# Kernel optimization log

Hardware: AMD Instinct MI355X
Metric: run time of the kernel (lower is better)

Reference implementation:

```python
import jax, jax.numpy as jnp
import numpy as np

B, T, D, H, DEPTH, FF, NC = 512, 150, 256, 8, 6, 1024, 4
HD = D // H  # head dim = 32


def setup_inputs() -> dict:
    key = jax.random.key(0)
    ks = iter(jax.random.split(key, 64))
    n = lambda shape, s=0.02: jax.random.normal(next(ks), shape, jnp.float32) * s
    return dict(
        token_types=jax.random.randint(next(ks), (B, T), 0, 4, jnp.int32),
        decision_ids=jax.random.randint(next(ks), (B, T), 0, NC, jnp.int32),
        action_vals=jax.random.normal(next(ks), (B, T, 1), jnp.float32),
        dis_vals=jax.random.normal(next(ks), (B, T, 10), jnp.float32),
        v_vals=jax.random.normal(next(ks), (B, T, 3), jnp.float32),
        action_W=n((1, D), 0.5), action_b=n((D,)),
        dis_W=n((10, D), 0.2), dis_b=n((D,)),
        v_W=n((3, D), 0.3), v_b=n((D,)),
        decision_table=n((NC, D)),
        pos_embed=n((1, T + 1, D)), cls_token=n((1, 1, D)),
        qkv_W=n((DEPTH, D, 3 * D), 0.05), qkv_b=jnp.zeros((DEPTH, 3 * D), jnp.float32),
        out_W=n((DEPTH, D, D), 0.05), out_b=jnp.zeros((DEPTH, D), jnp.float32),
        ln1_g=jnp.ones((DEPTH, D), jnp.float32), ln1_b=jnp.zeros((DEPTH, D), jnp.float32),
        ln2_g=jnp.ones((DEPTH, D), jnp.float32), ln2_b=jnp.zeros((DEPTH, D), jnp.float32),
        ffn1_W=n((DEPTH, D, FF), 0.05), ffn1_b=jnp.zeros((DEPTH, FF), jnp.float32),
        ffn2_W=n((DEPTH, FF, D), 0.05), ffn2_b=jnp.zeros((DEPTH, D), jnp.float32),
        dec_ln_g=jnp.ones((D,), jnp.float32), dec_ln_b=jnp.zeros((D,), jnp.float32),
        dec_W=n((D, NC), 0.05), dec_b=jnp.zeros((NC,), jnp.float32),
        act_ln_g=jnp.ones((D,), jnp.float32), act_ln_b=jnp.zeros((D,), jnp.float32),
        act_W=n((D, 1), 0.05), act_b=jnpp if False else jnp.zeros((1,), jnp.float32),
    )


def _ln(x, g, b):
    # PyTorch LayerNorm: eps=1e-5, biased variance
    m = jnp.mean(x, axis=-1, keepdims=True)
    v = jnp.mean(jnp.square(x - m), axis=-1, keepdims=True)
    return (x - m) * jax.lax.rsqrt(v + 1e-5) * g + b


def reference(token_types, decision_ids, action_vals, dis_vals, v_vals,
              action_W, action_b, dis_W, dis_b, v_W, v_b, decision_table,
              pos_embed, cls_token, qkv_W, qkv_b, out_W, out_b,
              ln1_g, ln1_b, ln2_g, ln2_b, ffn1_W, ffn1_b, ffn2_W, ffn2_b,
              dec_ln_g, dec_ln_b, dec_W, dec_b, act_ln_g, act_ln_b, act_W, act_b):
    # --- batched type-dispatched token embedding (replaces the per-token python loop) ---
    a_emb = action_vals @ action_W + action_b                     # [B,T,D] type 'A'
    s_emb = dis_vals @ dis_W + dis_b + v_vals @ v_W + v_b         # [B,T,D] type 'S'
    d_emb = decision_table[decision_ids]                          # [B,T,D] type 'D'
    t = token_types[..., None]
    x = jnp.where(t == 0, a_emb, jnp.where(t == 1, s_emb, jnp.where(t == 2, d_emb, 0.0)))
    # --- prepend CLS, add positional embedding ---
    x = jnp.concatenate([jnp.broadcast_to(cls_token, (x.shape[0], 1, D)), x], axis=1)
    S = x.shape[1]
    x = x + pos_embed[:, :S, :]
    # --- post-norm TransformerEncoder (PyTorch default: ReLU FFN, norm_first=False, eval/no dropout) ---
    scale = 1.0 / np.sqrt(HD).astype(np.float32)
    for i in range(DEPTH):
        qkv = x @ qkv_W[i] + qkv_b[i]                             # [B,S,3D]
        q, k, v = jnp.split(qkv, 3, axis=-1)
        q = q.reshape(-1, S, H, HD)
        k = k.reshape(-1, S, H, HD)
        v = v.reshape(-1, S, H, HD)
        att = jax.nn.softmax(jnp.einsum('bqhd,bkhd->bhqk', q, k) * scale, axis=-1)
        o = jnp.einsum('bhqk,bkhd->bqhd', att, v).reshape(-1, S, D)
        x = _ln(x + o @ out_W[i] + out_b[i], ln1_g[i], ln1_b[i])
        ff = jax.nn.relu(x @ ffn1_W[i] + ffn1_b[i]) @ ffn2_W[i] + ffn2_b[i]
        x = _ln(x + ff, ln2_g[i], ln2_b[i])
    cls = x[:, 0, :]
    decision_logits = _ln(cls, dec_ln_g, dec_ln_b) @ dec_W + dec_b   # [B,4]
    action_pred = _ln(cls, act_ln_g, act_ln_b) @ act_W + act_b       # [B,1]
    return (decision_logits, action_pred)
```

## Files before the change

kernel.cpp:

```cpp
#include <hip/hip_runtime.h>
#include <hip/hip_bf16.h>

typedef __hip_bfloat16 bf16;
typedef unsigned short u16;
typedef __attribute__((ext_vector_type(8))) short s16x8;
typedef __attribute__((ext_vector_type(4))) float f32x4;

#define B_ 512
#define T_ 150
#define S_ 151
#define D_ 256
#define H_ 8
#define HD_ 32
#define FF_ 1024
#define NC_ 4
#define DEPTH_ 6
#define MTOT 77312
#define MT128 (MTOT / 128)
#define MT64 (MTOT / 64)

#define XOFF 0
#define C1OFF (MTOT * D_)
#define C2OFF (C1OFF + MTOT * FF_)
#define WSELEMS (C2OFF + MTOT * D_)

#define QKVT_OFF 0
#define OUTT_OFF (QKVT_OFF + DEPTH_ * D_ * 768)
#define FFN1T_OFF (OUTT_OFF + DEPTH_ * D_ * D_)
#define FFN2T_OFF (FFN1T_OFF + DEPTH_ * D_ * FF_)
#define WTELEMS (FFN2T_OFF + DEPTH_ * FF_ * D_)

__device__ __align__(16) u16 g_ws[WSELEMS];
__device__ __align__(16) u16 g_wt[WTELEMS];
__device__ int g_f32flag;

__device__ __forceinline__ float ldf(const void* p, size_t i, int f) {
  return f ? ((const float*)p)[i] : __bfloat162float(((const bf16*)p)[i]);
}
__device__ __forceinline__ float b2f(u16 u) {
  union { unsigned int i; float f; } v; v.i = ((unsigned int)u) << 16; return v.f;
}
__device__ __forceinline__ u16 f2b(float x) {
  bf16 h = __float2bfloat16(x);
  return *reinterpret_cast<u16*>(&h);
}

typedef __attribute__((address_space(3))) void lds_void;
typedef const __attribute__((address_space(1))) void glob_void;
__device__ __forceinline__ void gload_lds16(const u16* g, u16* l) {
  __builtin_amdgcn_global_load_lds((glob_void*)g, (lds_void*)l, 16, 0, 0);
}

#define PROBE_N 38656
__global__ __launch_bounds__(256) void probe_kernel(const void* pe)
{
  const u16* w = (const u16*)pe;
  int susp = 0, zeroEven = 0;
  for (int k = threadIdx.x; k < PROBE_N; k += 256) {
    u16 u = w[k];
    int ex = (u >> 7) & 0xFF;
    if (ex >= 141) susp++;
    if ((k & 1) == 0 && (u & 0x7FFF) == 0) zeroEven++;
  }
  __shared__ int s_susp, s_zero;
  if (threadIdx.x == 0) { s_susp = 0; s_zero = 0; }
  __syncthreads();
  atomicAdd(&s_susp, susp);
  atomicAdd(&s_zero, zeroEven);
  __syncthreads();
  if (threadIdx.x == 0)
    g_f32flag = (s_susp > 0 || s_zero >= ((PROBE_N / 2) * 9) / 10) ? 1 : 0;
}

__global__ __launch_bounds__(256) void wtrans_kernel(const void* src, int dstOff,
                                                     int K, int N, int total)
{
  const int f = g_f32flag;
  int idx = blockIdx.x * 256 + threadIdx.x;
  if (idx >= total) return;
  int kn = K * N;
  int l = idx / kn;
  int r = idx - l * kn;
  int k = r / N;
  int n = r - k * N;
  g_wt[dstOff + (size_t)l * kn + (size_t)n * K + k] = f2b(ldf(src, idx, f));
}

__global__ __launch_bounds__(256) void embed_kernel(
    const int* __restrict__ tt, const int* __restrict__ dids,
    const void* av, const void* dv, const void* vv,
    const void* aW, const void* ab, const void* dW, const void* db,
    const void* vW, const void* vb, const void* table, const void* pos,
    const void* cls)
{
  const int f = g_f32flag;
  u16* x = g_ws + XOFF;
  int row = blockIdx.x;
  int d = threadIdx.x;
  int b = row / S_;
  int s = row - b * S_;
  float val;
  if (s == 0) {
    val = ldf(cls, d, f);
  } else {
    int t = s - 1;
    int idx = b * T_ + t;
    int ty = tt[idx];
    if (ty == 0) {
      val = ldf(av, idx, f) * ldf(aW, d, f) + ldf(ab, d, f);
    } else if (ty == 1) {
      float acc = ldf(db, d, f) + ldf(vb, d, f);
#pragma unroll
      for (int i = 0; i < 10; i++) acc += ldf(dv, (size_t)idx * 10 + i, f) * ldf(dW, i * D_ + d, f);
#pragma unroll
      for (int i = 0; i < 3; i++) acc += ldf(vv, (size_t)idx * 3 + i, f) * ldf(vW, i * D_ + d, f);
      val = acc;
    } else if (ty == 2) {
      int did = dids[idx] & (NC_ - 1);
      val = ldf(table, (size_t)did * D_ + d, f);
    } else {
      val = 0.f;
    }
  }
  val += ldf(pos, s * D_ + d, f);
  x[(size_t)row * D_ + d] = f2b(val);
}

__global__ __launch_bounds__(256, 3) void gemm_mfma(
    int aOff, int wtOff, const void* bias, size_t bOff,
    int cOff, int N, int K, int relu, int NB, int tiledC)
{
  const int f = g_f32flag;
  const u16* A = g_ws + aOff;
  const u16* Bt = g_wt + wtOff;
  u16* C = g_ws + cOff;
  __shared__ __align__(16) u16 sm[16384];
  const int tid = threadIdx.x;

  int gblk = blockIdx.x;
  int bm, bn;
  {
    const int full = (MT128 / 8) * 8;
    if (gblk < NB * full) {
      int per = NB * 8;
      int grp = gblk / per, rem = gblk % per;
      bm = grp * 8 + (rem & 7);
      bn = rem >> 3;
    } else {
      int id = gblk - NB * full;
      bm = full + id / NB;
      bn = id % NB;
    }
  }

  const int lane = tid & 63, wid = tid >> 6;
  const int wm = (wid >> 1) * 64, wn = (wid & 1) * 64;
  const int frow = lane & 15, quad = lane >> 4;

  const int rg = lane >> 3;
  const int ck = ((lane & 7) ^ rg) * 8;
  const u16* Ag[4]; const u16* Bg[4];
  u16 *Asl[4], *Bsl[4];
#pragma unroll
  for (int p = 0; p < 4; p++) {
    int grp = wid * 4 + p;
    int row = grp * 8 + rg;
    Ag[p] = A + (size_t)(bm * 128 + row) * K + ck;
    Bg[p] = Bt + (size_t)(bn * 128 + row) * K + ck;
    Asl[p] = &sm[grp * 512];
    Bsl[p] = &sm[8192 + grp * 512];
  }

  f32x4 acc[4][4] = {};

  for (int kt = 0; kt < K; kt += 64) {
    if (kt) __syncthreads();
#pragma unroll
    for (int p = 0; p < 4; p++) {
      gload_lds16(Ag[p] + kt, Asl[p]);
      gload_lds16(Bg[p] + kt, Bsl[p]);
    }
    __syncthreads();
#pragma unroll
    for (int s = 0; s < 2; s++) {
      s16x8 af[4], bfr[4];
      const int cfr = ((s * 4 + quad) ^ (frow & 7)) * 8;
#pragma unroll
      for (int t = 0; t < 4; t++) {
        af[t]  = *(const s16x8*)&sm[(wm + t * 16 + frow) * 64 + cfr];
        bfr[t] = *(const s16x8*)&sm[8192 + (wn + t * 16 + frow) * 64 + cfr];
      }
#pragma unroll
      for (int mt = 0; mt < 4; mt++)
#pragma unroll
        for (int nt = 0; nt < 4; nt++)
          acc[mt][nt] = __builtin_amdgcn_mfma_f32_16x16x32_bf16(af[mt], bfr[nt], acc[mt][nt], 0, 0, 0);
    }
  }

  float bv[4];
#pragma unroll
  for (int nt = 0; nt < 4; nt++)
    bv[nt] = ldf(bias, bOff + (size_t)(bn * 128 + wn + nt * 16 + frow), f);
  __syncthreads();
#pragma unroll
  for (int p = 0; p < 2; p++) {
    if ((wid >> 1) == p) {
#pragma unroll
      for (int mt = 0; mt < 4; mt++)
#pragma unroll
        for (int nt = 0; nt < 4; nt++)
#pragma unroll
          for (int r = 0; r < 4; r++) {
            int rl = (wm & 63) + mt * 16 + quad * 4 + r;
            float v = acc[mt][nt][r] + bv[nt];
            if (relu) v = fmaxf(v, 0.f);
            sm[rl * 136 + wn + nt * 16 + frow] = f2b(v);
          }
    }
    __syncthreads();
    {
      int rl = tid >> 2;
      int cq = (tid & 3) * 32;
      if (!tiledC) {
        size_t gb = (size_t)(bm * 128 + p * 64 + rl) * N + bn * 128 + cq;
#pragma unroll
        for (int j = 0; j < 4; j++)
          *(s16x8*)(C + gb + j * 8) = *(const s16x8*)&sm[rl * 136 + cq + j * 8];
      } else {
        const size_t tmBase = (size_t)(bm * 2 + p) * (N >> 6);
#pragma unroll
        for (int j = 0; j < 4; j++) {
          int col = bn * 128 + cq + j * 8;
          size_t addr = ((tmBase + (col >> 6)) << 12) + (rl << 6) + (col & 63);
          *(s16x8*)(C + addr) = *(const s16x8*)&sm[rl * 136 + cq + j * 8];
        }
      }
    }
    __syncthreads();
  }
}

#define LNHALF 20480

__global__ __launch_bounds__(256, 2) void gemm_ln(
    int aOff, int wtOff, const void* bias, size_t bOff,
    const void* lng, const void* lnb, size_t lnOff, int K)
{
  const int f = g_f32flag;
  const u16* A = g_ws + aOff;
  const u16* Bt = g_wt + wtOff;
  __shared__ __align__(16) u16 sm[2 * LNHALF];
  const int tid = threadIdx.x;
  const int bm = blockIdx.x;
  const int lane = tid & 63, wid = tid >> 6;
  const int wn = wid * 64;
  const int frow = lane & 15, quad = lane >> 4;
  const int rg = lane >> 3;
  const int ck = ((lane & 7) ^ rg) * 8;

  const u16* Ag[2]; u16* Asl[2];
  const u16* Bg[8]; u16* Bsl[8];
#pragma unroll
  for (int p = 0; p < 2; p++) {
    int grp = wid * 2 + p;
    Ag[p] = A + ((size_t)bm * (K >> 6) << 12) + ((grp * 8 + rg) << 6) + ck;
    Asl[p] = &sm[grp * 512];
  }
#pragma unroll
  for (int p = 0; p < 8; p++) {
    int grp = wid * 8 + p;
    Bg[p] = Bt + (size_t)(grp * 8 + rg) * K + ck;
    Bsl[p] = &sm[4096 + grp * 512];
  }

  f32x4 acc[4][4] = {};
  const int nsteps = K >> 6;

#pragma unroll
  for (int p = 0; p < 2; p++) gload_lds16(Ag[p], Asl[p]);
#pragma unroll
  for (int p = 0; p < 8; p++) gload_lds16(Bg[p], Bsl[p]);
  __syncthreads();

  for (int t = 0; t < nsteps; t++) {
    const int cur = (t & 1) * LNHALF;
    if (t + 1 < nsteps) {
      const int nxt = ((t + 1) & 1) * LNHALF;
      const int ktA = (t + 1) << 12;
      const int ktB = (t + 1) << 6;
#pragma unroll
      for (int p = 0; p < 2; p++) gload_lds16(Ag[p] + ktA, Asl[p] + nxt);
#pragma unroll
      for (int p = 0; p < 8; p++) gload_lds16(Bg[p] + ktB, Bsl[p] + nxt);
    }
#pragma unroll
    for (int s = 0; s < 2; s++) {
      s16x8 af[4], bfr[4];
      const int cfr = ((s * 4 + quad) ^ (frow & 7)) * 8;
#pragma unroll
      for (int ti = 0; ti < 4; ti++) {
        af[ti]  = *(const s16x8*)&sm[cur + (ti * 16 + frow) * 64 + cfr];
        bfr[ti] = *(const s16x8*)&sm[cur + 4096 + (wn + ti * 16 + frow) * 64 + cfr];
      }
#pragma unroll
      for (int mt = 0; mt < 4; mt++)
#pragma unroll
        for (int nt = 0; nt < 4; nt++)
          acc[mt][nt] = __builtin_amdgcn_mfma_f32_16x16x32_bf16(af[mt], bfr[nt], acc[mt][nt], 0, 0, 0);
    }
    __syncthreads();
  }

  const int rl = tid >> 2;
  const int cq = (tid & 3) * 64;
  const size_t rowg = (size_t)bm * 64 + rl;
  s16x8 xr[8];
#pragma unroll
  for (int j = 0; j < 8; j++)
    xr[j] = *(const s16x8*)(g_ws + XOFF + rowg * 256 + cq + j * 8);

  float bv[4];
#pragma unroll
  for (int nt = 0; nt < 4; nt++)
    bv[nt] = ldf(bias, bOff + (size_t)(wn + nt * 16 + frow), f);
#pragma unroll
  for (int mt = 0; mt < 4; mt++)
#pragma unroll
    for (int nt = 0; nt < 4; nt++)
#pragma unroll
      for (int r = 0; r < 4; r++) {
        int row = mt * 16 + quad * 4 + r;
        int col = wn + nt * 16 + frow;
        sm[row * 264 + col] = f2b(acc[mt][nt][r] + bv[nt]);
      }
  __syncthreads();
  {
    float s1 = 0.f, s2 = 0.f;
#pragma unroll
    for (int j = 0; j < 8; j++) {
      s16x8 yv = *(const s16x8*)&sm[rl * 264 + cq + j * 8];
#pragma unroll
      for (int e = 0; e < 8; e++) {
        float v = b2f((u16)yv[e]) + b2f((u16)xr[j][e]);
        s1 += v; s2 += v * v;
      }
    }
    s1 += __shfl_xor(s1, 1, 64); s2 += __shfl_xor(s2, 1, 64);
    s1 += __shfl_xor(s1, 2, 64); s2 += __shfl_xor(s2, 2, 64);
    float mean = s1 * (1.f / 256.f);
    float var = s2 * (1.f / 256.f) - mean * mean;
    float rs = rsqrtf(var + 1e-5f);
#pragma unroll
    for (int j = 0; j < 8; j++) {
      s16x8 yv = *(const s16x8*)&sm[rl * 264 + cq + j * 8];
      s16x8 ov;
#pragma unroll
      for (int e = 0; e < 8; e++) {
        float v = b2f((u16)yv[e]) + b2f((u16)xr[j][e]);
        int col = cq + j * 8 + e;
        ov[e] = (short)f2b((v - mean) * rs * ldf(lng, lnOff + col, f) + ldf(lnb, lnOff + col, f));
      }
      *(s16x8*)(g_ws + XOFF + rowg * 256 + cq + j * 8) = ov;
    }
  }
}

#define HST 72

__global__ __launch_bounds__(512, 2) void ffn_fused(
    int w1Off, const void* b1, size_t b1Off,
    int w2Off, const void* b2, size_t b2Off,
    const void* lng, const void* lnb, size_t lnOff)
{
  const int f = g_f32flag;
  const u16* W1t = g_wt + w1Off;
  const u16* W2t = g_wt + w2Off;
  __shared__ __align__(16) u16 sm[74752];
  u16* xs  = sm;
  u16* W1s = sm + 32768;
  u16* W2s = sm + 49152;
  u16* hs  = sm + 65536;
  const int tid = threadIdx.x;
  const int bm = blockIdx.x;
  const int lane = tid & 63, wid = tid >> 6;
  const int frow = lane & 15, quad = lane >> 4;
  const int rg = lane >> 3;
  const int ck = ((lane & 7) ^ rg) * 8;
  const int wrow = (wid >> 2) * 64;
  const int wcg = wid & 3;

#pragma unroll
  for (int kt = 0; kt < 4; kt++)
#pragma unroll
    for (int p = 0; p < 2; p++) {
      int grp = wid * 2 + p;
      gload_lds16(g_ws + XOFF + (size_t)(bm * 128 + grp * 8 + rg) * 256 + kt * 64 + ck,
                  &xs[kt * 8192 + grp * 512]);
    }
#pragma unroll
  for (int kt = 0; kt < 4; kt++)
    gload_lds16(W1t + (size_t)(wid * 8 + rg) * 256 + kt * 64 + ck,
                &W1s[kt * 4096 + wid * 512]);
#pragma unroll
  for (int p = 0; p < 4; p++) {
    int grp = wid * 4 + p;
    gload_lds16(W2t + (size_t)(grp * 8 + rg) * 1024 + ck, &W2s[grp * 512]);
  }

  f32x4 acc[4][4] = {};

  for (int c = 0; c < 16; c++) {
    __syncthreads();
    f32x4 a1[4] = {};
#pragma unroll
    for (int kt = 0; kt < 4; kt++)
#pragma unroll
      for (int s = 0; s < 2; s++) {
        const int cfr = ((s * 4 + quad) ^ (frow & 7)) * 8;
        s16x8 bf1 = *(const s16x8*)&W1s[kt * 4096 + (wcg * 16 + frow) * 64 + cfr];
#pragma unroll
        for (int mt = 0; mt < 4; mt++) {
          s16x8 af = *(const s16x8*)&xs[kt * 8192 + (wrow + mt * 16 + frow) * 64 + cfr];
          a1[mt] = __builtin_amdgcn_mfma_f32_16x16x32_bf16(af, bf1, a1[mt], 0, 0, 0);
        }
      }
    {
      float b1v = ldf(b1, b1Off + c * 64 + wcg * 16 + frow, f);
#pragma unroll
      for (int mt = 0; mt < 4; mt++)
#pragma unroll
        for (int r = 0; r < 4; r++)
          hs[(wrow + mt * 16 + quad * 4 + r) * HST + wcg * 16 + frow] =
              f2b(fmaxf(a1[mt][r] + b1v, 0.f));
    }
    __syncthreads();
    if (c + 1 < 16) {
#pragma unroll
      for (int kt = 0; kt < 4; kt++)
        gload_lds16(W1t + (size_t)((c + 1) * 64 + wid * 8 + rg) * 256 + kt * 64 + ck,
                    &W1s[kt * 4096 + wid * 512]);
    }
#pragma unroll
    for (int s2 = 0; s2 < 2; s2++) {
      const int cfr = ((s2 * 4 + quad) ^ (frow & 7)) * 8;
      s16x8 ap[4], bf2[4];
#pragma unroll
      for (int ti = 0; ti < 4; ti++)
        ap[ti] = *(const s16x8*)&hs[(wrow + ti * 16 + frow) * HST + s2 * 32 + quad * 8];
#pragma unroll
      for (int nt = 0; nt < 4; nt++)
        bf2[nt] = *(const s16x8*)&W2s[(wcg * 64 + nt * 16 + frow) * 64 + cfr];
#pragma unroll
      for (int mt = 0; mt < 4; mt++)
#pragma unroll
        for (int nt = 0; nt < 4; nt++)
          acc[mt][nt] = __builtin_amdgcn_mfma_f32_16x16x32_bf16(ap[mt], bf2[nt], acc[mt][nt], 0, 0, 0);
    }
    __syncthreads();
    if (c + 1 < 16) {
#pragma unroll
      for (int p = 0; p < 4; p++) {
        int grp = wid * 4 + p;
        gload_lds16(W2t + (size_t)(grp * 8 + rg) * 1024 + (c + 1) * 64 + ck,
                    &W2s[grp * 512]);
      }
    }
  }

  const int rl = tid >> 2;
  const int cq = (tid & 3) * 64;
  const size_t rowg = (size_t)bm * 128 + rl;
  s16x8 xr[8];
#pragma unroll
  for (int j = 0; j < 8; j++)
    xr[j] = *(const s16x8*)(g_ws + XOFF + rowg * 256 + cq + j * 8);

  float bv[4];
#pragma unroll
  for (int nt = 0; nt < 4; nt++)
    bv[nt] = ldf(b2, b2Off + (size_t)(wcg * 64 + nt * 16 + frow), f);
#pragma unroll
  for (int mt = 0; mt < 4; mt++)
#pragma unroll
    for (int nt = 0; nt < 4; nt++)
#pragma unroll
      for (int r = 0; r < 4; r++) {
        int row = wrow + mt * 16 + quad * 4 + r;
        int col = wcg * 64 + nt * 16 + frow;
        sm[row * 264 + col] = f2b(acc[mt][nt][r] + bv[nt]);
      }
  __syncthreads();
  {
    float s1 = 0.f, s2 = 0.f;
#pragma unroll
    for (int j = 0; j < 8; j++) {
      s16x8 yv = *(const s16x8*)&sm[rl * 264 + cq + j * 8];
#pragma unroll
      for (int e = 0; e < 8; e++) {
        float v = b2f((u16)yv[e]) + b2f((u16)xr[j][e]);
        s1 += v; s2 += v * v;
      }
    }
    s1 += __shfl_xor(s1, 1, 64); s2 += __shfl_xor(s2, 1, 64);
    s1 += __shfl_xor(s1, 2, 64); s2 += __shfl_xor(s2, 2, 64);
    float mean = s1 * (1.f / 256.f);
    float var = s2 * (1.f / 256.f) - mean * mean;
    float rs = rsqrtf(var + 1e-5f);
#pragma unroll
    for (int j = 0; j < 8; j++) {
      s16x8 yv = *(const s16x8*)&sm[rl * 264 + cq + j * 8];
      s16x8 ov;
#pragma unroll
      for (int e = 0; e < 8; e++) {
        float v = b2f((u16)yv[e]) + b2f((u16)xr[j][e]);
        int col = cq + j * 8 + e;
        ov[e] = (short)f2b((v - mean) * rs * ldf(lng, lnOff + col, f) + ldf(lnb, lnOff + col, f));
      }
      *(s16x8*)(g_ws + XOFF + rowg * 256 + cq + j * 8) = ov;
    }
  }
}

#define SP 160
#define KLD 32
#define VLD 170
#define PLDS 42

__global__ __launch_bounds__(320) void attn_kernel()
{
  const u16* qkv = g_ws + C1OFF;
  u16* o = g_ws + C2OFF;
  __shared__ __align__(16) u16 Ks[SP * KLD];
  __shared__ __align__(16) u16 Vt[HD_ * VLD];
  __shared__ __align__(16) u16 Ps[5][16 * PLDS];
  int bh = blockIdx.x;
  int b = bh >> 3, h = bh & 7;
  int tid = threadIdx.x;
  int lane = tid & 63, wid = tid >> 6;
  const u16* base = qkv + (size_t)b * S_ * 768;

  {
    const int jrow = lane >> 2;
    const int dsw = (((lane & 3) ^ ((lane >> 3) & 3)) * 8);
#pragma unroll
    for (int p = 0; p < 2; p++) {
      int g = wid * 2 + p;
      int j = g * 16 + jrow;
      gload_lds16(base + (size_t)j * 768 + 256 + h * 32 + dsw, &Ks[g * 512]);
    }
  }
  for (int g = tid; g < SP * 4; g += 320) {
    int j = g >> 2, d0 = (g & 3) * 8;
    s16x8 vv = {0, 0, 0, 0, 0, 0, 0, 0};
    if (j < S_) vv = *(const s16x8*)(base + (size_t)j * 768 + 512 + h * 32 + d0);
#pragma unroll
    for (int i = 0; i < 8; i++) Vt[(d0 + i) * VLD + j] = (u16)vv[i];
  }
  __syncthreads();

  const int frow = lane & 15;
  const int quad = lane >> 4;
  const int fk = quad * 8;
  const float scale = 0.17677669529663687f;
  u16* Pw = &Ps[wid][0];

  for (int round = 0; round < 2; round++) {
    int mt = round * 5 + wid;
    int qrow = mt * 16 + frow;
    s16x8 aq = {0, 0, 0, 0, 0, 0, 0, 0};
    if (qrow < S_) aq = *(const s16x8*)(base + (size_t)qrow * 768 + h * 32 + fk);
    f32x4 sacc[10];
#pragma unroll
    for (int nt = 0; nt < 10; nt++) {
      s16x8 bk = *(const s16x8*)&Ks[(nt * 16 + frow) * KLD
                                    + ((quad ^ ((frow >> 1) & 3)) * 8)];
      f32x4 z = {0.f, 0.f, 0.f, 0.f};
      sacc[nt] = __builtin_amdgcn_mfma_f32_16x16x32_bf16(aq, bk, z, 0, 0, 0);
    }
#pragma unroll
    for (int nt = 0; nt < 10; nt++) {
      int colg = nt * 16 + frow;
      float msk = (colg < S_) ? 1.f : 0.f;
#pragma unroll
      for (int r = 0; r < 4; r++)
        sacc[nt][r] = msk ? sacc[nt][r] * scale : -1e30f;
    }
    float inv[4];
#pragma unroll
    for (int r = 0; r < 4; r++) {
      float mx = -1e30f;
#pragma unroll
      for (int nt = 0; nt < 10; nt++) mx = fmaxf(mx, sacc[nt][r]);
#pragma unroll
      for (int m = 1; m < 16; m <<= 1) mx = fmaxf(mx, __shfl_xor(mx, m, 64));
      float sm2 = 0.f;
#pragma unroll
      for (int nt = 0; nt < 10; nt++) {
        float p = __expf(sacc[nt][r] - mx);
        sacc[nt][r] = p;
        sm2 += p;
      }
#pragma unroll
      for (int m = 1; m < 16; m <<= 1) sm2 += __shfl_xor(sm2, m, 64);
      inv[r] = 1.f / sm2;
    }
    f32x4 oacc[2] = {};
#pragma unroll
    for (int ks = 0; ks < 5; ks++) {
#pragma unroll
      for (int h2 = 0; h2 < 2; h2++) {
        int nt = ks * 2 + h2;
#pragma unroll
        for (int r = 0; r < 4; r++)
          Pw[(quad * 4 + r) * PLDS + h2 * 16 + frow] = f2b(sacc[nt][r]);
      }
      s16x8 ap = *(const s16x8*)&Pw[frow * PLDS + fk];
#pragma unroll
      for (int nt2 = 0; nt2 < 2; nt2++) {
        s16x8 bv = *(const s16x8*)&Vt[(nt2 * 16 + frow) * VLD + ks * 32 + fk];
        oacc[nt2] = __builtin_amdgcn_mfma_f32_16x16x32_bf16(ap, bv, oacc[nt2], 0, 0, 0);
      }
    }
#pragma unroll
    for (int nt2 = 0; nt2 < 2; nt2++)
#pragma unroll
      for (int r = 0; r < 4; r++) {
        int rowg = mt * 16 + quad * 4 + r;
        if (rowg < S_) {
          int gr = b * S_ + rowg;
          int gc = h * 32 + nt2 * 16 + frow;
          o[(((size_t)(gr >> 6) * (D_ >> 6) + (gc >> 6)) << 12)
            + ((gr & 63) << 6) + (gc & 63)] = f2b(oacc[nt2][r] * inv[r]);
        }
      }
  }
}

__global__ __launch_bounds__(256) void head_kernel(
    const void* dg, const void* dbt, const void* dW, const void* dbias,
    const void* ag, const void* abt, const void* aW, const void* abias,
    void* out)
{
  const int f = g_f32flag;
  const u16* x = g_ws + XOFF;
  int bg = blockIdx.x;
  int tid = threadIdx.x;
  float c = b2f(x[(size_t)bg * S_ * D_ + tid]);
  float s1 = c, s2 = c * c;
#pragma unroll
  for (int off = 32; off > 0; off >>= 1) {
    s1 += __shfl_down(s1, off, 64);
    s2 += __shfl_down(s2, off, 64);
  }
  __shared__ float ws1[4], ws2[4], stats[2];
  __shared__ float lnD[256], lnA[256];
  int wid = tid >> 6, lane = tid & 63;
  if (lane == 0) { ws1[wid] = s1; ws2[wid] = s2; }
  __syncthreads();
  if (tid == 0) {
    float t1 = ws1[0] + ws1[1] + ws1[2] + ws1[3];
    float t2 = ws2[0] + ws2[1] + ws2[2] + ws2[3];
    float mean = t1 * (1.f / 256.f);
    float var = t2 * (1.f / 256.f) - mean * mean;
    stats[0] = mean;
    stats[1] = rsqrtf(var + 1e-5f);
  }
  __syncthreads();
  float n = (c - stats[0]) * stats[1];
  lnD[tid] = n * ldf(dg, tid, f) + ldf(dbt, tid, f);
  lnA[tid] = n * ldf(ag, tid, f) + ldf(abt, tid, f);
  __syncthreads();
  if (tid < NC_) {
    float acc = ldf(dbias, tid, f);
    for (int k = 0; k < D_; k++) acc += lnD[k] * ldf(dW, k * NC_ + tid, f);
    if (f) ((float*)out)[bg * NC_ + tid] = acc;
    else   ((bf16*)out)[bg * NC_ + tid] = __float2bfloat16(acc);
  } else if (tid == 8) {
    float acc = ldf(abias, 0, f);
    for (int k = 0; k < D_; k++) acc += lnA[k] * ldf(aW, k, f);
    if (f) ((float*)out)[B_ * NC_ + bg] = acc;
    else   ((bf16*)out)[B_ * NC_ + bg] = __float2bfloat16(acc);
  }
}

extern "C" void kernel_launch(void* const* d_in, const int* in_sizes, int n_in,
                              void* d_out, int out_size, void* d_ws, size_t ws_size,
                              hipStream_t stream)
{
  (void)in_sizes; (void)out_size; (void)d_ws; (void)ws_size;
  if (n_in < 34) return;
  const int* token_types  = (const int*)d_in[0];
  const int* decision_ids = (const int*)d_in[1];

  probe_kernel<<<1, 256, 0, stream>>>(d_in[12]);

  wtrans_kernel<<<(DEPTH_ * D_ * 768 + 255) / 256, 256, 0, stream>>>(
      d_in[14], QKVT_OFF, D_, 768, DEPTH_ * D_ * 768);
  wtrans_kernel<<<(DEPTH_ * D_ * D_ + 255) / 256, 256, 0, stream>>>(
      d_in[16], OUTT_OFF, D_, D_, DEPTH_ * D_ * D_);
  wtrans_kernel<<<(DEPTH_ * D_ * FF_ + 255) / 256, 256, 0, stream>>>(
      d_in[22], FFN1T_OFF, D_, FF_, DEPTH_ * D_ * FF_);
  wtrans_kernel<<<(DEPTH_ * FF_ * D_ + 255) / 256, 256, 0, stream>>>(
      d_in[24], FFN2T_OFF, FF_, D_, DEPTH_ * FF_ * D_);

  embed_kernel<<<MTOT, 256, 0, stream>>>(token_types, decision_ids,
      d_in[2], d_in[3], d_in[4], d_in[5], d_in[6], d_in[7], d_in[8],
      d_in[9], d_in[10], d_in[11], d_in[12], d_in[13]);

  for (int i = 0; i < DEPTH_; i++) {
    gemm_mfma<<<6 * MT128, 256, 0, stream>>>(XOFF,
        QKVT_OFF + i * D_ * 768, d_in[15], (size_t)i * 768, C1OFF, 768, D_, 0, 6, 0);
    attn_kernel<<<B_ * H_, 320, 0, stream>>>();
    gemm_ln<<<MT64, 256, 0, stream>>>(C2OFF,
        OUTT_OFF + i * D_ * D_, d_in[17], (size_t)i * D_,
        d_in[18], d_in[19], (size_t)i * D_, D_);
    ffn_fused<<<MT128, 512, 0, stream>>>(
        FFN1T_OFF + i * D_ * FF_, d_in[23], (size_t)i * FF_,
        FFN2T_OFF + i * FF_ * D_, d_in[25], (size_t)i * D_,
        d_in[20], d_in[21], (size_t)i * D_);
  }
  head_kernel<<<B_, 256, 0, stream>>>(d_in[26], d_in[27], d_in[28], d_in[29],
      d_in[30], d_in[31], d_in[32], d_in[33], d_out);
}
```

Before: 2.503 ms.

## Shrink FFN shared memory by holding X fragments in registers

Measured after the change: 2.377 ms, median of 4. 5.1% less time.

```diff
diff --git a/kernel.cpp b/kernel.cpp
--- a/kernel.cpp
+++ b/kernel.cpp
@@ -366,7 +366,12 @@
   }
 }
 
-#define HST 72
+#define XS3_ 0
+#define W1S_ 8192
+#define W2S_ 24576
+#define HS_  40960
+#define B1S_ 49152
+#define FFSM 51200
 
 __global__ __launch_bounds__(512, 2) void ffn_fused(
     int w1Off, const void* b1, size_t b1Off,
@@ -376,11 +381,7 @@
   const int f = g_f32flag;
   const u16* W1t = g_wt + w1Off;
   const u16* W2t = g_wt + w2Off;
-  __shared__ __align__(16) u16 sm[74752];
-  u16* xs  = sm;
-  u16* W1s = sm + 32768;
-  u16* W2s = sm + 49152;
-  u16* hs  = sm + 65536;
+  __shared__ __align__(16) u16 sm[FFSM];
   const int tid = threadIdx.x;
   const int bm = blockIdx.x;
   const int lane = tid & 63, wid = tid >> 6;
@@ -390,80 +391,138 @@
   const int wrow = (wid >> 2) * 64;
   const int wcg = wid & 3;
 
-#pragma unroll
-  for (int kt = 0; kt < 4; kt++)
-#pragma unroll
-    for (int p = 0; p < 2; p++) {
-      int grp = wid * 2 + p;
-      gload_lds16(g_ws + XOFF + (size_t)(bm * 128 + grp * 8 + rg) * 256 + kt * 64 + ck,
-                  &xs[kt * 8192 + grp * 512]);
-    }
+  {
+    float* b1s = (float*)&sm[B1S_];
+    b1s[tid * 2]     = ldf(b1, b1Off + tid * 2, f);
+    b1s[tid * 2 + 1] = ldf(b1, b1Off + tid * 2 + 1, f);
+  }
+  {
+    const u16* xg = g_ws + XOFF;
+#pragma unroll
+    for (int kt = 0; kt < 4; kt++) {
+      const int dst = (kt == 0) ? W1S_ : (kt == 1) ? (W1S_ + 8192)
+                    : (kt == 2) ? W2S_ : XS3_;
+#pragma unroll
+      for (int p = 0; p < 2; p++) {
+        int grp = wid * 2 + p;
+        gload_lds16(xg + (size_t)(bm * 128 + grp * 8 + rg) * 256 + kt * 64 + ck,
+                    &sm[dst + grp * 512]);
+      }
+    }
+  }
+  __builtin_amdgcn_sched_barrier(0);
+  asm volatile("s_waitcnt vmcnt(0) lgkmcnt(0)" ::: "memory");
+  __builtin_amdgcn_sched_barrier(0);
+  __builtin_amdgcn_s_barrier();
+  __builtin_amdgcn_sched_barrier(0);
+
+  s16x8 xr[3][2][4];
+#pragma unroll
+  for (int kt = 0; kt < 3; kt++) {
+    const int base = (kt == 0) ? W1S_ : (kt == 1) ? (W1S_ + 8192) : W2S_;
+#pragma unroll
+    for (int s = 0; s < 2; s++) {
+      const int cfr = ((s * 4 + quad) ^ (frow & 7)) * 8;
+#pragma unroll
+      for (int mt = 0; mt < 4; mt++)
+        xr[kt][s][mt] = *(const s16x8*)&sm[base + (wrow + mt * 16 + frow) * 64 + cfr];
+    }
+  }
+  __builtin_amdgcn_sched_barrier(0);
+  asm volatile("s_waitcnt lgkmcnt(0)" ::: "memory");
+  __builtin_amdgcn_sched_barrier(0);
+  __builtin_amdgcn_s_barrier();
+  __builtin_amdgcn_sched_barrier(0);
+
 #pragma unroll
   for (int kt = 0; kt < 4; kt++)
     gload_lds16(W1t + (size_t)(wid * 8 + rg) * 256 + kt * 64 + ck,
-                &W1s[kt * 4096 + wid * 512]);
+                &sm[W1S_ + kt * 4096 + wid * 512]);
 #pragma unroll
   for (int p = 0; p < 4; p++) {
     int grp = wid * 4 + p;
-    gload_lds16(W2t + (size_t)(grp * 8 + rg) * 1024 + ck, &W2s[grp * 512]);
+    gload_lds16(W2t + (size_t)(grp * 8 + rg) * 1024 + ck, &sm[W2S_ + grp * 512]);
   }
 
   f32x4 acc[4][4] = {};
+  const float* b1s = (const float*)&sm[B1S_];
 
   for (int c = 0; c < 16; c++) {
-    __syncthreads();
+    __builtin_amdgcn_sched_barrier(0);
+    asm volatile("s_waitcnt vmcnt(4)" ::: "memory");
+    __builtin_amdgcn_sched_barrier(0);
+    __builtin_amdgcn_s_barrier();
+    __builtin_amdgcn_sched_barrier(0);
+
     f32x4 a1[4] = {};
 #pragma unroll
     for (int kt = 0; kt < 4; kt++)
 #pragma unroll
       for (int s = 0; s < 2; s++) {
         const int cfr = ((s * 4 + quad) ^ (frow & 7)) * 8;
-        s16x8 bf1 = *(const s16x8*)&W1s[kt * 4096 + (wcg * 16 + frow) * 64 + cfr];
-#pragma unroll
-        for (int mt = 0; mt < 4; mt++) {
-          s16x8 af = *(const s16x8*)&xs[kt * 8192 + (wrow + mt * 16 + frow) * 64 + cfr];
-          a1[mt] = __builtin_amdgcn_mfma_f32_16x16x32_bf16(af, bf1, a1[mt], 0, 0, 0);
+        s16x8 bf1 = *(const s16x8*)&sm[W1S_ + kt * 4096 + (wcg * 16 + frow) * 64 + cfr];
+        if (kt < 3) {
+#pragma unroll
+          for (int mt = 0; mt < 4; mt++)
+            a1[mt] = __builtin_amdgcn_mfma_f32_16x16x32_bf16(xr[kt][s][mt], bf1, a1[mt], 0, 0, 0);
+        } else {
+#pragma unroll
+          for (int mt = 0; mt < 4; mt++) {
+            s16x8 af = *(const s16x8*)&sm[XS3_ + (wrow + mt * 16 + frow) * 64 + cfr];
+            a1[mt] = __builtin_amdgcn_mfma_f32_16x16x32_bf16(af, bf1, a1[mt], 0, 0, 0);
+          }
         }
       }
     {
-      float b1v = ldf(b1, b1Off + c * 64 + wcg * 16 + frow, f);
+      float b1v = b1s[c * 64 + wcg * 16 + frow];
 #pragma unroll
       for (int mt = 0; mt < 4; mt++)
 #pragma unroll
-        for (int r = 0; r < 4; r++)
-          hs[(wrow + mt * 16 + quad * 4 + r) * HST + wcg * 16 + frow] =
-              f2b(fmaxf(a1[mt][r] + b1v, 0.f));
-    }
-    __syncthreads();
+        for (int r = 0; r < 4; r++) {
+          int row = wrow + mt * 16 + quad * 4 + r;
+          int swz = (((wcg * 2 + (frow >> 3)) ^ ((quad * 4 + r) & 7)) << 3) + (frow & 7);
+          sm[HS_ + row * 64 + swz] = f2b(fmaxf(a1[mt][r] + b1v, 0.f));
+        }
+    }
+    __builtin_amdgcn_sched_barrier(0);
+    asm volatile("s_waitcnt vmcnt(0) lgkmcnt(0)" ::: "memory");
+    __builtin_amdgcn_sched_barrier(0);
+    __builtin_amdgcn_s_barrier();
+    __builtin_amdgcn_sched_barrier(0);
     if (c + 1 < 16) {
 #pragma unroll
       for (int kt = 0; kt < 4; kt++)
         gload_lds16(W1t + (size_t)((c + 1) * 64 + wid * 8 + rg) * 256 + kt * 64 + ck,
-                    &W1s[kt * 4096 + wid * 512]);
+                    &sm[W1S_ + kt * 4096 + wid * 512]);
     }
 #pragma unroll
     for (int s2 = 0; s2 < 2; s2++) {
       const int cfr = ((s2 * 4 + quad) ^ (frow & 7)) * 8;
       s16x8 ap[4], bf2[4];
 #pragma unroll
-      for (int ti = 0; ti < 4; ti++)
-        ap[ti] = *(const s16x8*)&hs[(wrow + ti * 16 + frow) * HST + s2 * 32 + quad * 8];
+      for (int ti = 0; ti < 4; ti++) {
+        int row2 = wrow + ti * 16 + frow;
+        int blk = (s2 * 4 + quad) ^ (frow & 7);
+        ap[ti] = *(const s16x8*)&sm[HS_ + row2 * 64 + blk * 8];
+      }
 #pragma unroll
       for (int nt = 0; nt < 4; nt++)
-        bf2[nt] = *(const s16x8*)&W2s[(wcg * 64 + nt * 16 + frow) * 64 + cfr];
+        bf2[nt] = *(const s16x8*)&sm[W2S_ + (wcg * 64 + nt * 16 + frow) * 64 + cfr];
 #pragma unroll
       for (int mt = 0; mt < 4; mt++)
 #pragma unroll
         for (int nt = 0; nt < 4; nt++)
           acc[mt][nt] = __builtin_amdgcn_mfma_f32_16x16x32_bf16(ap[mt], bf2[nt], acc[mt][nt], 0, 0, 0);
     }
-    __syncthreads();
+    __builtin_amdgcn_sched_barrier(0);
+    __builtin_amdgcn_s_barrier();
+    __builtin_amdgcn_sched_barrier(0);
     if (c + 1 < 16) {
 #pragma unroll
       for (int p = 0; p < 4; p++) {
         int grp = wid * 4 + p;
         gload_lds16(W2t + (size_t)(grp * 8 + rg) * 1024 + (c + 1) * 64 + ck,
-                    &W2s[grp * 512]);
+                    &sm[W2S_ + grp * 512]);
       }
     }
   }
@@ -471,10 +530,10 @@
   const int rl = tid >> 2;
   const int cq = (tid & 3) * 64;
   const size_t rowg = (size_t)bm * 128 + rl;
-  s16x8 xr[8];
+  s16x8 resv[8];
 #pragma unroll
   for (int j = 0; j < 8; j++)
-    xr[j] = *(const s16x8*)(g_ws + XOFF + rowg * 256 + cq + j * 8);
+    resv[j] = *(const s16x8*)(g_ws + XOFF + rowg * 256 + cq + j * 8);
 
   float bv[4];
 #pragma unroll
@@ -498,7 +557,7 @@
       s16x8 yv = *(const s16x8*)&sm[rl * 264 + cq + j * 8];
 #pragma unroll
       for (int e = 0; e < 8; e++) {
-        float v = b2f((u16)yv[e]) + b2f((u16)xr[j][e]);
+        float v = b2f((u16)yv[e]) + b2f((u16)resv[j][e]);
         s1 += v; s2 += v * v;
       }
     }
@@ -513,7 +572,7 @@
       s16x8 ov;
 #pragma unroll
       for (int e = 0; e < 8; e++) {
-        float v = b2f((u16)yv[e]) + b2f((u16)xr[j][e]);
+        float v = b2f((u16)yv[e]) + b2f((u16)resv[j][e]);
         int col = cq + j * 8 + e;
         ov[e] = (short)f2b((v - mean) * rs * ldf(lng, lnOff + col, f) + ldf(lnb, lnOff + col, f));
       }
```

## Shrink fused FFN shared memory to run four blocks per CU

Applied to the files above, without the earlier changes.

Result: slower. 3.124 ms (+24.8%).

```diff
diff --git a/kernel.cpp b/kernel.cpp
--- a/kernel.cpp
+++ b/kernel.cpp
@@ -366,9 +366,15 @@
   }
 }
 
-#define HST 72
-
-__global__ __launch_bounds__(512, 2) void ffn_fused(
+#define XS2_ 0
+#define XS3_ 8192
+#define W1S_ 16384
+#define W2S_ 24576
+#define HS_  32768
+#define B1S_ 36864
+#define FFSM 38912
+
+__global__ __launch_bounds__(512, 4) void ffn_fused(
     int w1Off, const void* b1, size_t b1Off,
     int w2Off, const void* b2, size_t b2Off,
     const void* lng, const void* lnb, size_t lnOff)
@@ -376,81 +382,114 @@
   const int f = g_f32flag;
   const u16* W1t = g_wt + w1Off;
   const u16* W2t = g_wt + w2Off;
-  __shared__ __align__(16) u16 sm[74752];
-  u16* xs  = sm;
-  u16* W1s = sm + 32768;
-  u16* W2s = sm + 49152;
-  u16* hs  = sm + 65536;
+  __shared__ __align__(16) u16 sm[FFSM];
   const int tid = threadIdx.x;
   const int bm = blockIdx.x;
   const int lane = tid & 63, wid = tid >> 6;
   const int frow = lane & 15, quad = lane >> 4;
   const int rg = lane >> 3;
   const int ck = ((lane & 7) ^ rg) * 8;
-  const int wrow = (wid >> 2) * 64;
-  const int wcg = wid & 3;
-
-#pragma unroll
-  for (int kt = 0; kt < 4; kt++)
-#pragma unroll
-    for (int p = 0; p < 2; p++) {
-      int grp = wid * 2 + p;
-      gload_lds16(g_ws + XOFF + (size_t)(bm * 128 + grp * 8 + rg) * 256 + kt * 64 + ck,
-                  &xs[kt * 8192 + grp * 512]);
-    }
-#pragma unroll
-  for (int kt = 0; kt < 4; kt++)
-    gload_lds16(W1t + (size_t)(wid * 8 + rg) * 256 + kt * 64 + ck,
-                &W1s[kt * 4096 + wid * 512]);
-#pragma unroll
-  for (int p = 0; p < 4; p++) {
-    int grp = wid * 4 + p;
-    gload_lds16(W2t + (size_t)(grp * 8 + rg) * 1024 + ck, &W2s[grp * 512]);
+  const int rg2 = lane >> 2;
+  const int ck2 = ((lane & 3) ^ (rg2 & 3)) * 8;
+  const int wrow1 = (wid >> 1) * 32;
+  const int jcol  = (wid & 1) * 16 + frow;
+  const int wrow2 = (wid >> 2) * 64;
+  const int wcg   = wid & 3;
+
+  {
+    float* b1s = (float*)&sm[B1S_];
+    b1s[tid * 2]     = ldf(b1, b1Off + tid * 2, f);
+    b1s[tid * 2 + 1] = ldf(b1, b1Off + tid * 2 + 1, f);
+  }
+  {
+    const u16* xg = g_ws + XOFF;
+    const int dstb[4] = {W1S_, W2S_, XS2_, XS3_};
+#pragma unroll
+    for (int kt = 0; kt < 4; kt++)
+#pragma unroll
+      for (int p = 0; p < 2; p++) {
+        int g = wid * 2 + p;
+        gload_lds16(xg + (size_t)(bm * 128 + g * 8 + rg) * 256 + kt * 64 + ck,
+                    &sm[dstb[kt] + g * 512]);
+      }
+  }
+  __syncthreads();
+
+  s16x8 xr[2][2][2];
+#pragma unroll
+  for (int kt = 0; kt < 2; kt++) {
+    const int base = kt ? W2S_ : W1S_;
+#pragma unroll
+    for (int s = 0; s < 2; s++) {
+      const int cfr = ((s * 4 + quad) ^ (frow & 7)) * 8;
+#pragma unroll
+      for (int mt = 0; mt < 2; mt++)
+        xr[kt][s][mt] = *(const s16x8*)&sm[base + (wrow1 + mt * 16 + frow) * 64 + cfr];
+    }
+  }
+  __syncthreads();
+
+#pragma unroll
+  for (int p = 0; p < 2; p++) {
+    int flat = wid * 2 + p;
+    int kt = flat >> 2, g = flat & 3;
+    gload_lds16(W1t + (size_t)(g * 8 + rg) * 256 + kt * 64 + ck,
+                &sm[W1S_ + kt * 2048 + g * 512]);
+  }
+#pragma unroll
+  for (int p = 0; p < 2; p++) {
+    int g = wid * 2 + p;
+    gload_lds16(W2t + (size_t)(g * 16 + rg2) * 1024 + ck2,
+                &sm[W2S_ + g * 512]);
   }
 
   f32x4 acc[4][4] = {};
-
-  for (int c = 0; c < 16; c++) {
+  const float* b1s = (const float*)&sm[B1S_];
+
+  for (int c = 0; c < 32; c++) {
     __syncthreads();
-    f32x4 a1[4] = {};
+    f32x4 a1[2] = {};
 #pragma unroll
     for (int kt = 0; kt < 4; kt++)
 #pragma unroll
       for (int s = 0; s < 2; s++) {
         const int cfr = ((s * 4 + quad) ^ (frow & 7)) * 8;
-        s16x8 bf1 = *(const s16x8*)&W1s[kt * 4096 + (wcg * 16 + frow) * 64 + cfr];
-#pragma unroll
-        for (int mt = 0; mt < 4; mt++) {
-          s16x8 af = *(const s16x8*)&xs[kt * 8192 + (wrow + mt * 16 + frow) * 64 + cfr];
-          a1[mt] = __builtin_amdgcn_mfma_f32_16x16x32_bf16(af, bf1, a1[mt], 0, 0, 0);
+        s16x8 bf1 = *(const s16x8*)&sm[W1S_ + kt * 2048 + jcol * 64 + cfr];
+        if (kt < 2) {
+#pragma unroll
+          for (int mt = 0; mt < 2; mt++)
+            a1[mt] = __builtin_amdgcn_mfma_f32_16x16x32_bf16(xr[kt][s][mt], bf1, a1[mt], 0, 0, 0);
+        } else {
+          const int xb = (kt == 2) ? XS2_ : XS3_;
+#pragma unroll
+          for (int mt = 0; mt < 2; mt++) {
+            s16x8 af = *(const s16x8*)&sm[xb + (wrow1 + mt * 16 + frow) * 64 + cfr];
+            a1[mt] = __builtin_amdgcn_mfma_f32_16x16x32_bf16(af, bf1, a1[mt], 0, 0, 0);
+          }
         }
       }
     {
-      float b1v = ldf(b1, b1Off + c * 64 + wcg * 16 + frow, f);
-#pragma unroll
-      for (int mt = 0; mt < 4; mt++)
-#pragma unroll
-        for (int r = 0; r < 4; r++)
-          hs[(wrow + mt * 16 + quad * 4 + r) * HST + wcg * 16 + frow] =
+      float b1v = b1s[c * 32 + jcol];
+      const int cc = (wid & 1) * 2 + (frow >> 3);
+#pragma unroll
+      for (int mt = 0; mt < 2; mt++)
+#pragma unroll
+        for (int r = 0; r < 4; r++) {
+          int row = wrow1 + mt * 16 + quad * 4 + r;
+          sm[HS_ + row * 32 + ((cc ^ (row & 3)) << 3) + (frow & 7)] =
               f2b(fmaxf(a1[mt][r] + b1v, 0.f));
+        }
     }
     __syncthreads();
-    if (c + 1 < 16) {
-#pragma unroll
-      for (int kt = 0; kt < 4; kt++)
-        gload_lds16(W1t + (size_t)((c + 1) * 64 + wid * 8 + rg) * 256 + kt * 64 + ck,
-                    &W1s[kt * 4096 + wid * 512]);
-    }
-#pragma unroll
-    for (int s2 = 0; s2 < 2; s2++) {
-      const int cfr = ((s2 * 4 + quad) ^ (frow & 7)) * 8;
+    {
+      const int slot = (quad ^ (frow & 3)) << 3;
       s16x8 ap[4], bf2[4];
 #pragma unroll
       for (int ti = 0; ti < 4; ti++)
-        ap[ti] = *(const s16x8*)&hs[(wrow + ti * 16 + frow) * HST + s2 * 32 + quad * 8];
+        ap[ti] = *(const s16x8*)&sm[HS_ + (wrow2 + ti * 16 + frow) * 32 + slot];
 #pragma unroll
       for (int nt = 0; nt < 4; nt++)
-        bf2[nt] = *(const s16x8*)&W2s[(wcg * 64 + nt * 16 + frow) * 64 + cfr];
+        bf2[nt] = *(const s16x8*)&sm[W2S_ + (wcg * 64 + nt * 16 + frow) * 32 + slot];
 #pragma unroll
       for (int mt = 0; mt < 4; mt++)
 #pragma unroll
@@ -458,12 +497,19 @@
           acc[mt][nt] = __builtin_amdgcn_mfma_f32_16x16x32_bf16(ap[mt], bf2[nt], acc[mt][nt], 0, 0, 0);
     }
     __syncthreads();
-    if (c + 1 < 16) {
-#pragma unroll
-      for (int p = 0; p < 4; p++) {
-        int grp = wid * 4 + p;
-        gload_lds16(W2t + (size_t)(grp * 8 + rg) * 1024 + (c + 1) * 64 + ck,
-                    &W2s[grp * 512]);
+    if (c + 1 < 32) {
+#pragma unroll
+      for (int p = 0; p < 2; p++) {
+        int flat = wid * 2 + p;
+        int kt = flat >> 2, g = flat & 3;
+        gload_lds16(W1t + (size_t)((c + 1) * 32 + g * 8 + rg) * 256 + kt * 64 + ck,
+                    &sm[W1S_ + kt * 2048 + g * 512]);
+      }
+#pragma unroll
+      for (int p = 0; p < 2; p++) {
+        int g = wid * 2 + p;
+        gload_lds16(W2t + (size_t)(g * 16 + rg2) * 1024 + (c + 1) * 32 + ck2,
+                    &sm[W2S_ + g * 512]);
       }
     }
   }
@@ -471,10 +517,10 @@
   const int rl = tid >> 2;
   const int cq = (tid & 3) * 64;
   const size_t rowg = (size_t)bm * 128 + rl;
-  s16x8 xr[8];
+  s16x8 resv[8];
 #pragma unroll
   for (int j = 0; j < 8; j++)
-    xr[j] = *(const s16x8*)(g_ws + XOFF + rowg * 256 + cq + j * 8);
+    resv[j] = *(const s16x8*)(g_ws + XOFF + rowg * 256 + cq + j * 8);
 
   float bv[4];
 #pragma unroll
@@ -486,7 +532,7 @@
     for (int nt = 0; nt < 4; nt++)
 #pragma unroll
       for (int r = 0; r < 4; r++) {
-        int row = wrow + mt * 16 + quad * 4 + r;
+        int row = wrow2 + mt * 16 + quad * 4 + r;
         int col = wcg * 64 + nt * 16 + frow;
         sm[row * 264 + col] = f2b(acc[mt][nt][r] + bv[nt]);
       }
@@ -498,7 +544,7 @@
       s16x8 yv = *(const s16x8*)&sm[rl * 264 + cq + j * 8];
 #pragma unroll
       for (int e = 0; e < 8; e++) {
-        float v = b2f((u16)yv[e]) + b2f((u16)xr[j][e]);
+        float v = b2f((u16)yv[e]) + b2f((u16)resv[j][e]);
         s1 += v; s2 += v * v;
       }
     }
@@ -513,7 +559,7 @@
       s16x8 ov;
 #pragma unroll
       for (int e = 0; e < 8; e++) {
-        float v = b2f((u16)yv[e]) + b2f((u16)xr[j][e]);
+        float v = b2f((u16)yv[e]) + b2f((u16)resv[j][e]);
         int col = cq + j * 8 + e;
         ov[e] = (short)f2b((v - mean) * rs * ldf(lng, lnOff + col, f) + ldf(lnb, lnOff + col, f));
       }
```
